# Kernel tuning notes

Hardware: AMD Instinct MI355X
Metric: run time of the kernel (lower is better)

## Reference

```python
import jax, jax.numpy as jnp
import numpy as np

NX, NY, D, K = 20000, 50000, 64, 8
NUM_BATCHES = 2


def _knn_np(px, py, bx, by, k):
    # Batched exact kNN via chunked squared-distance + argpartition (mirrors torch_cluster.knn under no_grad).
    pp = (px * px).sum(1)
    idx = np.empty((py.shape[0], k), np.int32)
    chunk = 4096
    for s in range(0, py.shape[0], chunk):
        q = py[s:s + chunk]
        d = (q * q).sum(1)[:, None] + pp[None, :] - 2.0 * (q @ px.T)
        d = np.where(by[s:s + chunk, None] == bx[None, :], d, np.inf)
        idx[s:s + chunk] = np.argpartition(d, k, axis=1)[:, :k].astype(np.int32)
    return idx


def setup_inputs() -> dict:
    rng = np.random.default_rng(0)
    pos_x = (rng.random((NX, 3)) * 10.0).astype(np.float32)
    pos_y = (rng.random((NY, 3)) * 10.0).astype(np.float32)
    bx = np.repeat(np.arange(NUM_BATCHES), NX // NUM_BATCHES).astype(np.int32)
    by = np.repeat(np.arange(NUM_BATCHES), NY // NUM_BATCHES).astype(np.int32)
    x_idx = _knn_np(pos_x, pos_y, bx, by, K).reshape(-1)            # [NY*K]
    y_idx = np.repeat(np.arange(NY, dtype=np.int32), K)             # [NY*K]

    key = jax.random.key(0)
    ks = jax.random.split(key, 6)

    def lin(k, fi, fo):
        return jax.random.normal(k, (fi, fo), jnp.float32) / np.sqrt(fi).astype(np.float32)

    return {
        "x": jax.random.normal(ks[0], (NX, D), jnp.float32),
        "pos_x": jnp.asarray(pos_x),
        "pos_y": jnp.asarray(pos_y),
        "x_idx": jnp.asarray(x_idx),
        "y_idx": jnp.asarray(y_idx),
        # ResnetBlockFC 1: size_in=D+3, size_h=D, size_out=D (shortcut linear, no bias)
        "W0a": lin(ks[1], D + 3, D), "b0a": jnp.zeros((D,), jnp.float32),
        "W1a": lin(ks[2], D, D),     "b1a": jnp.zeros((D,), jnp.float32),
        "Wsa": lin(ks[3], D + 3, D),
        # ResnetBlockFC 2: size_in=size_h=size_out=D (identity shortcut)
        "W0b": lin(ks[4], D, D),     "b0b": jnp.zeros((D,), jnp.float32),
        "W1b": lin(ks[5], D, D),     "b1b": jnp.zeros((D,), jnp.float32),
    }


def reference(x, pos_x, pos_y, x_idx, y_idx, W0a, b0a, W1a, b1a, Wsa, W0b, b0b, W1b, b1b):
    # gather + positional diff (diff computed under no_grad in the original)
    diff = jax.lax.stop_gradient(pos_x[x_idx] - pos_y[y_idx])        # [E, 3]
    h = jnp.concatenate([x[x_idx], diff], axis=1)                    # [E, D+3]
    # ResnetBlockFC 1: out = shortcut(h) + fc1(relu(fc0(relu(h))))
    net = jax.nn.relu(h) @ W0a + b0a
    dx = jax.nn.relu(net) @ W1a + b1a
    h = h @ Wsa + dx                                                 # [E, D]
    # ResnetBlockFC 2 (identity shortcut)
    net = jax.nn.relu(h) @ W0b + b0b
    h = h + jax.nn.relu(net) @ W1b + b1b                             # [E, D]
    # scatter-max back to query points (every query has exactly K edges)
    out = jax.ops.segment_max(h, y_idx, num_segments=NY)             # [NY, D]
    return out
```

## Files before the change

kernel.cpp:

```cpp
#include <hip/hip_runtime.h>


typedef _Float16 f16x8 __attribute__((ext_vector_type(8)));
typedef _Float16 f16x4 __attribute__((ext_vector_type(4)));
typedef float    f32x4 __attribute__((ext_vector_type(4)));

constexpr int NX     = 20000;
constexpr int NROWS  = 50000 * 8;
constexpr int NTILES = NROWS / 16;
constexpr int NFRAG  = 60;
constexpr int BW     = 8;
constexpr int BLOCK  = 64 * BW;
constexpr int TS2    = 72;

__global__ void prep_x(const float* __restrict__ x, _Float16* __restrict__ x16) {
    const int i = blockIdx.x * blockDim.x + threadIdx.x;
    if (i < NX * 16) {
        float4 v = ((const float4*)x)[i];
        f16x4 o = {(_Float16)v.x, (_Float16)v.y, (_Float16)v.z, (_Float16)v.w};
        *(f16x4*)(x16 + (size_t)i * 4) = o;
    }
}

static __device__ __forceinline__ void pack_relu(const f32x4* A, f16x8* bf) {
#pragma unroll
    for (int s = 0; s < 2; ++s) {
        f16x8 r;
#pragma unroll
        for (int e = 0; e < 8; ++e) {
            float v = A[2 * s + (e >> 2)][e & 3];
            r[e] = (_Float16)(v > 0.0f ? v : 0.0f);
        }
        bf[s] = r;
    }
}

__global__ __launch_bounds__(BLOCK, 4)
void pointnet_fused(const _Float16* __restrict__ x16,
                    const float* __restrict__ pos_x,
                    const float* __restrict__ pos_y,
                    const int*   __restrict__ x_idx,
                    const float* __restrict__ W0a, const float* __restrict__ b0a,
                    const float* __restrict__ W1a, const float* __restrict__ b1a,
                    const float* __restrict__ Wsa,
                    const float* __restrict__ W0b, const float* __restrict__ b0b,
                    const float* __restrict__ W1b, const float* __restrict__ b1b,
                    float* __restrict__ out)
{
    __shared__ __align__(16) _Float16 bfrag[NFRAG * 64 * 8];
    __shared__ __align__(16) _Float16 ebuf[BW][16 * TS2];

    const int tid = threadIdx.x;

    for (int p = tid; p < NFRAG * 64; p += BLOCK) {
        const int f = p >> 6, l = p & 63;
        const int q = l >> 4, n0 = l & 15;
        const int grp = f / 12, fl = f % 12, s = fl >> 2, t = fl & 3;
        const int col = t * 16 + n0;
        f16x8 v;
#pragma unroll
        for (int j = 0; j < 8; ++j) {
            const int k = 32 * s + 8 * q + j;
            float val = 0.0f;
            if (grp == 0)      val = (k < 67) ? W0a[k * 64 + col] : (k == 67 ? b0a[col] : 0.0f);
            else if (grp == 1) val = (k < 67) ? Wsa[k * 64 + col] : 0.0f;
            else {
                const float* W  = (grp == 2) ? W1a : (grp == 3) ? W0b : W1b;
                const float* bb = (grp == 2) ? b1a : (grp == 3) ? b0b : b1b;
                if (s < 2) {
                    const int row = 32 * s + 16 * (j >> 2) + 4 * q + (j & 3);
                    val = W[row * 64 + col];
                } else {
                    val = (q == 0 && j == 0) ? bb[col] : 0.0f;
                }
            }
            v[j] = (_Float16)val;
        }
        *(f16x8*)&bfrag[p * 8] = v;
    }
    __syncthreads();

    const int lane = tid & 63;
    const int wv   = tid >> 6;
    const int n0   = lane & 15;
    const int q    = lane >> 4;

    _Float16* eb = ebuf[wv];

    f16x8 bfr = {};
    if (q == 0) bfr[0] = (_Float16)1.0f;

    const int ey  = (lane >> 3) & 1;
    const int efg = lane & 7;
    const int esb = lane >> 4;

    const int gwave  = blockIdx.x * BW + wv;
    const int nwaves = gridDim.x * BW;

#define WFRAG(fid) (*(const f16x8*)&bfrag[(((fid) * 64) + lane) * 8])

    for (int tile = gwave; tile < NTILES; tile += nwaves) {
        const int row = tile * 16 + n0;
        const int xi  = x_idx[row];
        const _Float16* xp = x16 + (long)xi * 64 + q * 8;
        f16x8 hn[3];
        hn[0] = *(const f16x8*)(xp);
        hn[1] = *(const f16x8*)(xp + 32);
        {
            f16x8 z = {};
            hn[2] = z;
            if (q == 0) {
                const int yi = row >> 3;
#pragma unroll
                for (int j = 0; j < 3; ++j)
                    hn[2][j] = (_Float16)(pos_x[xi * 3 + j] - pos_y[yi * 3 + j]);
                hn[2][3] = (_Float16)1.0f;
            }
        }

        f32x4 A2[4];
#pragma unroll
        for (int t = 0; t < 4; ++t) A2[t] = (f32x4){0.f, 0.f, 0.f, 0.f};
#pragma unroll
        for (int s = 0; s < 3; ++s)
#pragma unroll
            for (int t = 0; t < 4; ++t)
                A2[t] = __builtin_amdgcn_mfma_f32_16x16x32_f16(WFRAG(12 + s * 4 + t), hn[s], A2[t], 0, 0, 0);

#pragma unroll
        for (int s = 0; s < 3; ++s)
#pragma unroll
            for (int j = 0; j < 8; ++j) {
                _Float16 v = hn[s][j];
                hn[s][j] = v > (_Float16)0 ? v : (_Float16)0;
            }
        f32x4 A1[4];
#pragma unroll
        for (int t = 0; t < 4; ++t) A1[t] = (f32x4){0.f, 0.f, 0.f, 0.f};
#pragma unroll
        for (int s = 0; s < 3; ++s)
#pragma unroll
            for (int t = 0; t < 4; ++t)
                A1[t] = __builtin_amdgcn_mfma_f32_16x16x32_f16(WFRAG(s * 4 + t), hn[s], A1[t], 0, 0, 0);

        f16x8 bf[2];
        pack_relu(A1, bf);
#pragma unroll
        for (int t = 0; t < 4; ++t) {
            A2[t] = __builtin_amdgcn_mfma_f32_16x16x32_f16(WFRAG(24 + 0 * 4 + t), bf[0], A2[t], 0, 0, 0);
            A2[t] = __builtin_amdgcn_mfma_f32_16x16x32_f16(WFRAG(24 + 1 * 4 + t), bf[1], A2[t], 0, 0, 0);
            A2[t] = __builtin_amdgcn_mfma_f32_16x16x32_f16(WFRAG(24 + 2 * 4 + t), bfr,   A2[t], 0, 0, 0);
        }

        pack_relu(A2, bf);
        f32x4 A3[4];
#pragma unroll
        for (int t = 0; t < 4; ++t) A3[t] = (f32x4){0.f, 0.f, 0.f, 0.f};
#pragma unroll
        for (int t = 0; t < 4; ++t) {
            A3[t] = __builtin_amdgcn_mfma_f32_16x16x32_f16(WFRAG(36 + 0 * 4 + t), bf[0], A3[t], 0, 0, 0);
            A3[t] = __builtin_amdgcn_mfma_f32_16x16x32_f16(WFRAG(36 + 1 * 4 + t), bf[1], A3[t], 0, 0, 0);
            A3[t] = __builtin_amdgcn_mfma_f32_16x16x32_f16(WFRAG(36 + 2 * 4 + t), bfr,   A3[t], 0, 0, 0);
        }

        pack_relu(A3, bf);
#pragma unroll
        for (int t = 0; t < 4; ++t) {
            A2[t] = __builtin_amdgcn_mfma_f32_16x16x32_f16(WFRAG(48 + 0 * 4 + t), bf[0], A2[t], 0, 0, 0);
            A2[t] = __builtin_amdgcn_mfma_f32_16x16x32_f16(WFRAG(48 + 1 * 4 + t), bf[1], A2[t], 0, 0, 0);
            A2[t] = __builtin_amdgcn_mfma_f32_16x16x32_f16(WFRAG(48 + 2 * 4 + t), bfr,   A2[t], 0, 0, 0);
        }

        __threadfence_block();
#pragma unroll
        for (int t = 0; t < 4; ++t) {
            f16x4 w;
#pragma unroll
            for (int r = 0; r < 4; ++r) w[r] = (_Float16)A2[t][r];
            *(f16x4*)&eb[n0 * TS2 + t * 16 + q * 4] = w;
        }
        __threadfence_block();

        const int dr0 = ey * 8 + esb * 2;
        f16x8 ra = *(const f16x8*)&eb[dr0 * TS2 + efg * 8];
        f16x8 rb = *(const f16x8*)&eb[(dr0 + 1) * TS2 + efg * 8];
#pragma unroll
        for (int e = 0; e < 8; ++e) ra[e] = ra[e] > rb[e] ? ra[e] : rb[e];
#pragma unroll
        for (int st = 0; st < 2; ++st) {
            union { f16x8 h; int i[4]; } u, v2;
            u.h = ra;
#pragma unroll
            for (int d = 0; d < 4; ++d) v2.i[d] = __shfl_xor(u.i[d], st == 0 ? 16 : 32, 64);
#pragma unroll
            for (int e = 0; e < 8; ++e) ra[e] = ra[e] > v2.h[e] ? ra[e] : v2.h[e];
        }
        if (esb == 0) {
            float4 f0 = {(float)ra[0], (float)ra[1], (float)ra[2], (float)ra[3]};
            float4 f1 = {(float)ra[4], (float)ra[5], (float)ra[6], (float)ra[7]};
            float* op = out + (long)(tile * 2 + ey) * 64 + efg * 8;
            *(float4*)op = f0;
            *(float4*)(op + 4) = f1;
        }
    }
#undef WFRAG
}

extern "C" void kernel_launch(void* const* d_in, const int* in_sizes, int n_in,
                              void* d_out, int out_size, void* d_ws, size_t ws_size,
                              hipStream_t stream) {
    (void)in_sizes; (void)n_in; (void)ws_size; (void)out_size;
    _Float16* x16 = (_Float16*)d_ws;

    prep_x<<<(NX * 16 + 255) / 256, 256, 0, stream>>>((const float*)d_in[0], x16);

    pointnet_fused<<<512, BLOCK, 0, stream>>>(
        x16,
        (const float*)d_in[1],
        (const float*)d_in[2],
        (const int*)  d_in[3],
        (const float*)d_in[5],  (const float*)d_in[6],
        (const float*)d_in[7],  (const float*)d_in[8],
        (const float*)d_in[9],
        (const float*)d_in[10], (const float*)d_in[11],
        (const float*)d_in[12], (const float*)d_in[13],
        (float*)d_out);
}
```

Before: 121.5 us.

## Process two 16-row tiles per wave and fold biases into accumulator init

Each wave now handles a pair of 16-edge tiles per iteration, so every weight fragment read from LDS feeds two MFMAs instead of one. The separate bias MFMA (a constant-one k-slice) is removed: biases for the three 64-wide layers go into a small LDS array and are used to initialise or add into the accumulators, shrinking the fragment table from 60 to 48 entries. Work is assigned statically, with a remainder pair handed to one wave per block, and the occupancy hint drops from 4 to 3 blocks to make room for the doubled register state. The cost is higher register pressure and fewer resident waves to hide gather latency.

```diff
diff --git a/kernel.cpp b/kernel.cpp
--- a/kernel.cpp
+++ b/kernel.cpp
@@ -7,10 +7,14 @@
 
 constexpr int NX     = 20000;
 constexpr int NROWS  = 50000 * 8;
-constexpr int NTILES = NROWS / 16;
-constexpr int NFRAG  = 60;
+constexpr int NPAIRS = NROWS / 32;
+constexpr int NFRAG  = 48;
 constexpr int BW     = 8;
 constexpr int BLOCK  = 64 * BW;
+constexpr int GRID   = 512;
+constexpr int NWAVES = GRID * BW;
+constexpr int FULLR  = NPAIRS / NWAVES;
+constexpr int REM    = NPAIRS - FULLR * NWAVES;
 constexpr int TS2    = 72;
 
 __global__ void prep_x(const float* __restrict__ x, _Float16* __restrict__ x16) {
@@ -35,7 +39,7 @@
     }
 }
 
-__global__ __launch_bounds__(BLOCK, 4)
+__global__ __launch_bounds__(BLOCK, 3)
 void pointnet_fused(const _Float16* __restrict__ x16,
                     const float* __restrict__ pos_x,
                     const float* __restrict__ pos_y,
@@ -49,13 +53,20 @@
 {
     __shared__ __align__(16) _Float16 bfrag[NFRAG * 64 * 8];
     __shared__ __align__(16) _Float16 ebuf[BW][16 * TS2];
+    __shared__ __align__(16) float bias_lds[3 * 64];
 
     const int tid = threadIdx.x;
 
     for (int p = tid; p < NFRAG * 64; p += BLOCK) {
         const int f = p >> 6, l = p & 63;
         const int q = l >> 4, n0 = l & 15;
-        const int grp = f / 12, fl = f % 12, s = fl >> 2, t = fl & 3;
+        int grp, fl;
+        if (f < 12)      { grp = 0; fl = f; }
+        else if (f < 24) { grp = 1; fl = f - 12; }
+        else if (f < 32) { grp = 2; fl = f - 24; }
+        else if (f < 40) { grp = 3; fl = f - 32; }
+        else             { grp = 4; fl = f - 40; }
+        const int s = fl >> 2, t = fl & 3;
         const int col = t * 16 + n0;
         f16x8 v;
 #pragma unroll
@@ -65,18 +76,18 @@
             if (grp == 0)      val = (k < 67) ? W0a[k * 64 + col] : (k == 67 ? b0a[col] : 0.0f);
             else if (grp == 1) val = (k < 67) ? Wsa[k * 64 + col] : 0.0f;
             else {
-                const float* W  = (grp == 2) ? W1a : (grp == 3) ? W0b : W1b;
-                const float* bb = (grp == 2) ? b1a : (grp == 3) ? b0b : b1b;
-                if (s < 2) {
-                    const int row = 32 * s + 16 * (j >> 2) + 4 * q + (j & 3);
-                    val = W[row * 64 + col];
-                } else {
-                    val = (q == 0 && j == 0) ? bb[col] : 0.0f;
-                }
+                const float* W = (grp == 2) ? W1a : (grp == 3) ? W0b : W1b;
+                const int row = 32 * s + 16 * (j >> 2) + 4 * q + (j & 3);
+                val = W[row * 64 + col];
             }
             v[j] = (_Float16)val;
         }
         *(f16x8*)&bfrag[p * 8] = v;
+    }
+    if (tid < 192) {
+        const int L = tid >> 6, i = tid & 63;
+        const float* b = (L == 0) ? b1a : (L == 1) ? b0b : b1b;
+        bias_lds[tid] = b[i];
     }
     __syncthreads();
 
@@ -87,120 +98,161 @@
 
     _Float16* eb = ebuf[wv];
 
-    f16x8 bfr = {};
-    if (q == 0) bfr[0] = (_Float16)1.0f;
-
     const int ey  = (lane >> 3) & 1;
     const int efg = lane & 7;
     const int esb = lane >> 4;
 
-    const int gwave  = blockIdx.x * BW + wv;
-    const int nwaves = gridDim.x * BW;
+    const int gwave = blockIdx.x * BW + wv;
+    const int extra = (blockIdx.x < REM && wv == (blockIdx.x & 7)) ? 1 : 0;
+    const int niter = FULLR + extra;
+    const int epair = FULLR * NWAVES + blockIdx.x;
 
 #define WFRAG(fid) (*(const f16x8*)&bfrag[(((fid) * 64) + lane) * 8])
 
-    for (int tile = gwave; tile < NTILES; tile += nwaves) {
-        const int row = tile * 16 + n0;
-        const int xi  = x_idx[row];
-        const _Float16* xp = x16 + (long)xi * 64 + q * 8;
-        f16x8 hn[3];
-        hn[0] = *(const f16x8*)(xp);
-        hn[1] = *(const f16x8*)(xp + 32);
-        {
+    for (int it = 0; it < niter; ++it) {
+        const int pair = (it < FULLR) ? (gwave + it * NWAVES) : epair;
+
+        f16x8 hn[2][3];
+#pragma unroll
+        for (int u = 0; u < 2; ++u) {
+            const int row = pair * 32 + u * 16 + n0;
+            const int xi  = x_idx[row];
+            const _Float16* xp = x16 + (long)xi * 64 + q * 8;
+            hn[u][0] = *(const f16x8*)(xp);
+            hn[u][1] = *(const f16x8*)(xp + 32);
             f16x8 z = {};
-            hn[2] = z;
+            hn[u][2] = z;
             if (q == 0) {
                 const int yi = row >> 3;
 #pragma unroll
                 for (int j = 0; j < 3; ++j)
-                    hn[2][j] = (_Float16)(pos_x[xi * 3 + j] - pos_y[yi * 3 + j]);
-                hn[2][3] = (_Float16)1.0f;
-            }
-        }
-
-        f32x4 A2[4];
-#pragma unroll
-        for (int t = 0; t < 4; ++t) A2[t] = (f32x4){0.f, 0.f, 0.f, 0.f};
+                    hn[u][2][j] = (_Float16)(pos_x[xi * 3 + j] - pos_y[yi * 3 + j]);
+                hn[u][2][3] = (_Float16)1.0f;
+            }
+        }
+
+        f32x4 A2[2][4];
+#pragma unroll
+        for (int t = 0; t < 4; ++t) {
+            const f32x4 bv = *(const f32x4*)&bias_lds[0 * 64 + t * 16 + q * 4];
+            A2[0][t] = bv;
+            A2[1][t] = bv;
+        }
 #pragma unroll
         for (int s = 0; s < 3; ++s)
 #pragma unroll
-            for (int t = 0; t < 4; ++t)
-                A2[t] = __builtin_amdgcn_mfma_f32_16x16x32_f16(WFRAG(12 + s * 4 + t), hn[s], A2[t], 0, 0, 0);
-
+            for (int t = 0; t < 4; ++t) {
+                const f16x8 w = WFRAG(12 + s * 4 + t);
+                A2[0][t] = __builtin_amdgcn_mfma_f32_16x16x32_f16(w, hn[0][s], A2[0][t], 0, 0, 0);
+                A2[1][t] = __builtin_amdgcn_mfma_f32_16x16x32_f16(w, hn[1][s], A2[1][t], 0, 0, 0);
+            }
+
+#pragma unroll
+        for (int u = 0; u < 2; ++u)
+#pragma unroll
+            for (int s = 0; s < 3; ++s)
+#pragma unroll
+                for (int j = 0; j < 8; ++j) {
+                    _Float16 v = hn[u][s][j];
+                    hn[u][s][j] = v > (_Float16)0 ? v : (_Float16)0;
+                }
+        f32x4 A1[2][4];
+#pragma unroll
+        for (int u = 0; u < 2; ++u)
+#pragma unroll
+            for (int t = 0; t < 4; ++t) A1[u][t] = (f32x4){0.f, 0.f, 0.f, 0.f};
 #pragma unroll
         for (int s = 0; s < 3; ++s)
 #pragma unroll
-            for (int j = 0; j < 8; ++j) {
-                _Float16 v = hn[s][j];
-                hn[s][j] = v > (_Float16)0 ? v : (_Float16)0;
-            }
-        f32x4 A1[4];
-#pragma unroll
-        for (int t = 0; t < 4; ++t) A1[t] = (f32x4){0.f, 0.f, 0.f, 0.f};
-#pragma unroll
-        for (int s = 0; s < 3; ++s)
-#pragma unroll
-            for (int t = 0; t < 4; ++t)
-                A1[t] = __builtin_amdgcn_mfma_f32_16x16x32_f16(WFRAG(s * 4 + t), hn[s], A1[t], 0, 0, 0);
-
-        f16x8 bf[2];
-        pack_relu(A1, bf);
+            for (int t = 0; t < 4; ++t) {
+                const f16x8 w = WFRAG(s * 4 + t);
+                A1[0][t] = __builtin_amdgcn_mfma_f32_16x16x32_f16(w, hn[0][s], A1[0][t], 0, 0, 0);
+                A1[1][t] = __builtin_amdgcn_mfma_f32_16x16x32_f16(w, hn[1][s], A1[1][t], 0, 0, 0);
+            }
+
+        f16x8 bf[2][2];
+        pack_relu(A1[0], bf[0]);
+        pack_relu(A1[1], bf[1]);
+#pragma unroll
+        for (int s = 0; s < 2; ++s)
+#pragma unroll
+            for (int t = 0; t < 4; ++t) {
+                const f16x8 w = WFRAG(24 + s * 4 + t);
+                A2[0][t] = __builtin_amdgcn_mfma_f32_16x16x32_f16(w, bf[0][s], A2[0][t], 0, 0, 0);
+                A2[1][t] = __builtin_amdgcn_mfma_f32_16x16x32_f16(w, bf[1][s], A2[1][t], 0, 0, 0);
+            }
+
+        pack_relu(A2[0], bf[0]);
+        pack_relu(A2[1], bf[1]);
+        f32x4 A3[2][4];
 #pragma unroll
         for (int t = 0; t < 4; ++t) {
-            A2[t] = __builtin_amdgcn_mfma_f32_16x16x32_f16(WFRAG(24 + 0 * 4 + t), bf[0], A2[t], 0, 0, 0);
-            A2[t] = __builtin_amdgcn_mfma_f32_16x16x32_f16(WFRAG(24 + 1 * 4 + t), bf[1], A2[t], 0, 0, 0);
-            A2[t] = __builtin_amdgcn_mfma_f32_16x16x32_f16(WFRAG(24 + 2 * 4 + t), bfr,   A2[t], 0, 0, 0);
-        }
-
-        pack_relu(A2, bf);
-        f32x4 A3[4];
-#pragma unroll
-        for (int t = 0; t < 4; ++t) A3[t] = (f32x4){0.f, 0.f, 0.f, 0.f};
+            const f32x4 bv = *(const f32x4*)&bias_lds[1 * 64 + t * 16 + q * 4];
+            A3[0][t] = bv;
+            A3[1][t] = bv;
+        }
+#pragma unroll
+        for (int s = 0; s < 2; ++s)
+#pragma unroll
+            for (int t = 0; t < 4; ++t) {
+                const f16x8 w = WFRAG(32 + s * 4 + t);
+                A3[0][t] = __builtin_amdgcn_mfma_f32_16x16x32_f16(w, bf[0][s], A3[0][t], 0, 0, 0);
+                A3[1][t] = __builtin_amdgcn_mfma_f32_16x16x32_f16(w, bf[1][s], A3[1][t], 0, 0, 0);
+            }
+
+        pack_relu(A3[0], bf[0]);
+        pack_relu(A3[1], bf[1]);
 #pragma unroll
         for (int t = 0; t < 4; ++t) {
-            A3[t] = __builtin_amdgcn_mfma_f32_16x16x32_f16(WFRAG(36 + 0 * 4 + t), bf[0], A3[t], 0, 0, 0);
-            A3[t] = __builtin_amdgcn_mfma_f32_16x16x32_f16(WFRAG(36 + 1 * 4 + t), bf[1], A3[t], 0, 0, 0);
-            A3[t] = __builtin_amdgcn_mfma_f32_16x16x32_f16(WFRAG(36 + 2 * 4 + t), bfr,   A3[t], 0, 0, 0);
-        }
-
-        pack_relu(A3, bf);
-#pragma unroll
-        for (int t = 0; t < 4; ++t) {
-            A2[t] = __builtin_amdgcn_mfma_f32_16x16x32_f16(WFRAG(48 + 0 * 4 + t), bf[0], A2[t], 0, 0, 0);
-            A2[t] = __builtin_amdgcn_mfma_f32_16x16x32_f16(WFRAG(48 + 1 * 4 + t), bf[1], A2[t], 0, 0, 0);
-            A2[t] = __builtin_amdgcn_mfma_f32_16x16x32_f16(WFRAG(48 + 2 * 4 + t), bfr,   A2[t], 0, 0, 0);
-        }
-
-        __threadfence_block();
-#pragma unroll
-        for (int t = 0; t < 4; ++t) {
-            f16x4 w;
-#pragma unroll
-            for (int r = 0; r < 4; ++r) w[r] = (_Float16)A2[t][r];
-            *(f16x4*)&eb[n0 * TS2 + t * 16 + q * 4] = w;
-        }
-        __threadfence_block();
-
-        const int dr0 = ey * 8 + esb * 2;
-        f16x8 ra = *(const f16x8*)&eb[dr0 * TS2 + efg * 8];
-        f16x8 rb = *(const f16x8*)&eb[(dr0 + 1) * TS2 + efg * 8];
-#pragma unroll
-        for (int e = 0; e < 8; ++e) ra[e] = ra[e] > rb[e] ? ra[e] : rb[e];
-#pragma unroll
-        for (int st = 0; st < 2; ++st) {
-            union { f16x8 h; int i[4]; } u, v2;
-            u.h = ra;
-#pragma unroll
-            for (int d = 0; d < 4; ++d) v2.i[d] = __shfl_xor(u.i[d], st == 0 ? 16 : 32, 64);
-#pragma unroll
-            for (int e = 0; e < 8; ++e) ra[e] = ra[e] > v2.h[e] ? ra[e] : v2.h[e];
-        }
-        if (esb == 0) {
-            float4 f0 = {(float)ra[0], (float)ra[1], (float)ra[2], (float)ra[3]};
-            float4 f1 = {(float)ra[4], (float)ra[5], (float)ra[6], (float)ra[7]};
-            float* op = out + (long)(tile * 2 + ey) * 64 + efg * 8;
-            *(float4*)op = f0;
-            *(float4*)(op + 4) = f1;
+            const f32x4 bv = *(const f32x4*)&bias_lds[2 * 64 + t * 16 + q * 4];
+#pragma unroll
+            for (int r = 0; r < 4; ++r) {
+                A2[0][t][r] += bv[r];
+                A2[1][t][r] += bv[r];
+            }
+        }
+#pragma unroll
+        for (int s = 0; s < 2; ++s)
+#pragma unroll
+            for (int t = 0; t < 4; ++t) {
+                const f16x8 w = WFRAG(40 + s * 4 + t);
+                A2[0][t] = __builtin_amdgcn_mfma_f32_16x16x32_f16(w, bf[0][s], A2[0][t], 0, 0, 0);
+                A2[1][t] = __builtin_amdgcn_mfma_f32_16x16x32_f16(w, bf[1][s], A2[1][t], 0, 0, 0);
+            }
+
+#pragma unroll
+        for (int u = 0; u < 2; ++u) {
+            __threadfence_block();
+#pragma unroll
+            for (int t = 0; t < 4; ++t) {
+                f16x4 w;
+#pragma unroll
+                for (int r = 0; r < 4; ++r) w[r] = (_Float16)A2[u][t][r];
+                *(f16x4*)&eb[n0 * TS2 + t * 16 + q * 4] = w;
+            }
+            __threadfence_block();
+
+            const int dr0 = ey * 8 + esb * 2;
+            f16x8 ra = *(const f16x8*)&eb[dr0 * TS2 + efg * 8];
+            f16x8 rb = *(const f16x8*)&eb[(dr0 + 1) * TS2 + efg * 8];
+#pragma unroll
+            for (int e = 0; e < 8; ++e) ra[e] = ra[e] > rb[e] ? ra[e] : rb[e];
+#pragma unroll
+            for (int st = 0; st < 2; ++st) {
+                union { f16x8 h; int i[4]; } uu, vv;
+                uu.h = ra;
+#pragma unroll
+                for (int d = 0; d < 4; ++d) vv.i[d] = __shfl_xor(uu.i[d], st == 0 ? 16 : 32, 64);
+#pragma unroll
+                for (int e = 0; e < 8; ++e) ra[e] = ra[e] > vv.h[e] ? ra[e] : vv.h[e];
+            }
+            if (esb == 0) {
+                float4 f0 = {(float)ra[0], (float)ra[1], (float)ra[2], (float)ra[3]};
+                float4 f1 = {(float)ra[4], (float)ra[5], (float)ra[6], (float)ra[7]};
+                float* op = out + (long)(pair * 4 + u * 2 + ey) * 64 + efg * 8;
+                *(float4*)op = f0;
+                *(float4*)(op + 4) = f1;
+            }
         }
     }
 #undef WFRAG
@@ -214,7 +266,7 @@
 
     prep_x<<<(NX * 16 + 255) / 256, 256, 0, stream>>>((const float*)d_in[0], x16);
 
-    pointnet_fused<<<512, BLOCK, 0, stream>>>(
+    pointnet_fused<<<GRID, BLOCK, 0, stream>>>(
         x16,
         (const float*)d_in[1],
         (const float*)d_in[2],
```

New measurement: 124.0 us. +2.1%, slower.
